# Kernel optimization log

Measured on AMD Instinct MI355X. Metric: run time of the kernel, lower is better.

## Reference

```python
import jax, jax.numpy as jnp
import numpy as np

N_EMBD = 1024
N_HEAD = 16
HEAD = N_EMBD // N_HEAD
B, T = 4, 2048


def setup_inputs() -> dict:
    key = jax.random.key(0)
    k1, k2, k3, k4, k5 = jax.random.split(key, 5)
    s = 1.0 / np.sqrt(N_EMBD)
    x = jax.random.normal(k1, (B, T, N_EMBD), dtype=jnp.float32)
    W_qkv = jax.random.uniform(k2, (N_EMBD, 3 * N_EMBD), jnp.float32, -s, s)
    b_qkv = jax.random.uniform(k3, (3 * N_EMBD,), jnp.float32, -s, s)
    W_out = jax.random.uniform(k4, (N_EMBD, N_EMBD), jnp.float32, -s, s)
    b_out = jax.random.uniform(k5, (N_EMBD,), jnp.float32, -s, s)
    return {"x": x, "W_qkv": W_qkv, "b_qkv": b_qkv, "W_out": W_out, "b_out": b_out}


def reference(x, W_qkv, b_qkv, W_out, b_out):
    Bx, Tx, C = x.shape
    qkv = x @ W_qkv + b_qkv                      # [B,T,3C]
    q, k, v = jnp.split(qkv, 3, axis=-1)
    def to_heads(t):
        return t.reshape(Bx, Tx, N_HEAD, HEAD).transpose(0, 2, 1, 3)  # [B,H,T,hd]
    q, k, v = to_heads(q), to_heads(k), to_heads(v)
    scores = jnp.einsum('bhqd,bhkd->bhqk', q, k) / np.sqrt(HEAD)
    causal = jnp.tril(jnp.ones((Tx, Tx), dtype=bool))
    scores = jnp.where(causal[None, None, :, :], scores, jnp.float32(-1e9))
    attn = jax.nn.softmax(scores, axis=-1)       # dropout p=0 (eval)
    out = jnp.einsum('bhqk,bhkd->bhqd', attn, v)
    out = out.transpose(0, 2, 1, 3).reshape(Bx, Tx, C)
    return out @ W_out + b_out
```

## Files before the change

kernel.cpp:

```cpp
#include <hip/hip_runtime.h>

typedef __attribute__((ext_vector_type(8))) short short8;
typedef __attribute__((ext_vector_type(8))) _Float16 half8;
typedef __attribute__((ext_vector_type(4))) float f32x4;
typedef __attribute__((ext_vector_type(16))) float f32x16;

#define MFMA_BF16(a, b, c) __builtin_amdgcn_mfma_f32_16x16x32_bf16(a, b, c, 0, 0, 0)
#define MFMA32_BF16(a, b, c) __builtin_amdgcn_mfma_f32_32x32x16_bf16(a, b, c, 0, 0, 0)
#define MFMA32_F16(a, b, c) __builtin_amdgcn_mfma_f32_32x32x16_f16(a, b, c, 0, 0, 0)

#define GLD16(g, l)                                                          \
  __builtin_amdgcn_global_load_lds(                                          \
      (const __attribute__((address_space(1))) unsigned int*)(g),            \
      (__attribute__((address_space(3))) unsigned int*)(l), 16, 0, 0)

__device__ __forceinline__ unsigned short f2bf(float f) {
  unsigned int u = __float_as_uint(f);
  u += 0x7fffu + ((u >> 16) & 1u);
  return (unsigned short)(u >> 16);
}

__global__ __launch_bounds__(256) void cvt_f32_bf16_k(const float* __restrict__ in,
                                                      unsigned short* __restrict__ out,
                                                      int n4) {
  int i = blockIdx.x * 256 + threadIdx.x;
  if (i < n4) {
    float4 v = reinterpret_cast<const float4*>(in)[i];
    ushort4 o;
    o.x = f2bf(v.x); o.y = f2bf(v.y); o.z = f2bf(v.z); o.w = f2bf(v.w);
    reinterpret_cast<ushort4*>(out)[i] = o;
  }
}

__global__ __launch_bounds__(256) void transpose_cvt_k(const float* __restrict__ W,
                                                       unsigned short* __restrict__ Wt,
                                                       int N) {
  __shared__ float tile[64][65];
  const int tid = threadIdx.x;
  const int tk = blockIdx.x * 64;
  const int tn = blockIdx.y * 64;
#pragma unroll
  for (int c = 0; c < 4; ++c) {
    int k = c * 16 + (tid >> 4);
    int n = (tid & 15) * 4;
    float4 v = *reinterpret_cast<const float4*>(&W[(size_t)(tk + k) * N + tn + n]);
    tile[k][n] = v.x; tile[k][n + 1] = v.y; tile[k][n + 2] = v.z; tile[k][n + 3] = v.w;
  }
  __syncthreads();
#pragma unroll
  for (int p = 0; p < 2; ++p) {
    int n = p * 32 + (tid >> 3);
    int k = (tid & 7) * 8;
    ushort4 a, b;
    a.x = f2bf(tile[k + 0][n]); a.y = f2bf(tile[k + 1][n]);
    a.z = f2bf(tile[k + 2][n]); a.w = f2bf(tile[k + 3][n]);
    b.x = f2bf(tile[k + 4][n]); b.y = f2bf(tile[k + 5][n]);
    b.z = f2bf(tile[k + 6][n]); b.w = f2bf(tile[k + 7][n]);
    *reinterpret_cast<ushort4*>(&Wt[(size_t)(tn + n) * 1024 + tk + k]) = a;
    *reinterpret_cast<ushort4*>(&Wt[(size_t)(tn + n) * 1024 + tk + k + 4]) = b;
  }
}

template <int MODE, int BN>
__global__ __launch_bounds__(256) void gemm_bt(const unsigned short* __restrict__ A,
                                               const unsigned short* __restrict__ Bt,
                                               const float* __restrict__ bias,
                                               float* __restrict__ outF,
                                               unsigned short* __restrict__ q_ws,
                                               unsigned short* __restrict__ k_ws,
                                               unsigned short* __restrict__ vt_ws,
                                               int M, int N, int K) {
  constexpr int NJ = BN / 32;
  constexpr int NBC = BN * 64 / 2048;
  __shared__ unsigned short As[128 * 64];
  __shared__ unsigned short Bs[BN * 64];

  const int tid = threadIdx.x;
  const int wave = tid >> 6, lane = tid & 63;
  const int quad = lane >> 4, l15 = lane & 15;
  const int m0 = blockIdx.x * 128, n0 = blockIdx.y * BN;
  const int wm = (wave & 1) * 64, wn = (wave >> 1) * (BN / 2);

  const f32x4 zf = {0.f, 0.f, 0.f, 0.f};
  f32x4 acc[4][NJ];
#pragma unroll
  for (int i = 0; i < 4; ++i)
#pragma unroll
    for (int j = 0; j < NJ; ++j) acc[i][j] = zf;

  const int rr = tid >> 3;
  const int scol = ((tid & 7) ^ (rr & 7)) * 8;
  const int swz = l15 & 7;

  for (int kt = 0; kt < K; kt += 64) {
    __syncthreads();
#pragma unroll
    for (int c = 0; c < 4; ++c)
      GLD16(&A[(size_t)(m0 + c * 32 + rr) * K + kt + scol], &As[c * 2048 + tid * 8]);
#pragma unroll
    for (int c = 0; c < NBC; ++c)
      GLD16(&Bt[(size_t)(n0 + c * 32 + rr) * K + kt + scol], &Bs[c * 2048 + tid * 8]);
    __syncthreads();

#pragma unroll
    for (int kk = 0; kk < 2; ++kk) {
      const int ch = (kk * 4 + quad) ^ swz;
      short8 af[4], bg[NJ];
#pragma unroll
      for (int i = 0; i < 4; ++i)
        af[i] = *reinterpret_cast<const short8*>(&As[(wm + i * 16 + l15) * 64 + ch * 8]);
#pragma unroll
      for (int j = 0; j < NJ; ++j)
        bg[j] = *reinterpret_cast<const short8*>(&Bs[(wn + j * 16 + l15) * 64 + ch * 8]);
#pragma unroll
      for (int i = 0; i < 4; ++i)
#pragma unroll
        for (int j = 0; j < NJ; ++j) acc[i][j] = MFMA_BF16(af[i], bg[j], acc[i][j]);
    }
  }

  const float kScQ = 0.125f * 1.44269504088896f;
  const int cls = n0 >> 10;
#pragma unroll
  for (int i = 0; i < 4; ++i) {
#pragma unroll
    for (int j = 0; j < NJ; ++j) {
      const int n = n0 + wn + j * 16 + l15;
      const float bv = bias[n];
      const int mb = m0 + wm + i * 16 + quad * 4;
      if (MODE == 1) {
#pragma unroll
        for (int r = 0; r < 4; ++r) outF[(size_t)(mb + r) * N + n] = acc[i][j][r] + bv;
      } else if (cls == 0) {
        const int b = mb >> 11, t0 = mb & 2047;
        const int h = n >> 6, d = n & 63;
#pragma unroll
        for (int r = 0; r < 4; ++r)
          q_ws[(((size_t)(b * 16 + h)) * 2048 + t0 + r) * 64 + d] =
              f2bf((acc[i][j][r] + bv) * kScQ);
      } else if (cls == 1) {
        const int b = mb >> 11, t0 = mb & 2047;
        const int n2 = n - 1024, h = n2 >> 6, d = n2 & 63;
#pragma unroll
        for (int r = 0; r < 4; ++r)
          k_ws[(((size_t)(b * 16 + h)) * 2048 + t0 + r) * 64 + d] = f2bf(acc[i][j][r] + bv);
      } else {
        const int b = mb >> 11, t0 = mb & 2047;
        const int n2 = n - 2048, h = n2 >> 6, d = n2 & 63;
        uint2 pk;
        pk.x = __builtin_bit_cast(unsigned int,
                                  __builtin_amdgcn_cvt_pkrtz(acc[i][j][0] + bv, acc[i][j][1] + bv));
        pk.y = __builtin_bit_cast(unsigned int,
                                  __builtin_amdgcn_cvt_pkrtz(acc[i][j][2] + bv, acc[i][j][3] + bv));
        *reinterpret_cast<uint2*>(
            &vt_ws[(((size_t)(b * 16 + h)) * 64 + d) * 2048 + t0]) = pk;
      }
    }
  }
}

__global__ __launch_bounds__(256, 3) void attn_k(const unsigned short* __restrict__ q_ws,
                                                 const unsigned short* __restrict__ k_ws,
                                                 const unsigned short* __restrict__ vt_ws,
                                                 unsigned short* __restrict__ att_ws) {
  const int T = 2048;
  const int bid = blockIdx.x;
  const int bh = (bid & 7) * 8 + ((bid >> 3) & 7);
  const int s = 15 - (bid >> 6);
  const int tid = threadIdx.x;
  const int wv = tid >> 6, lane = tid & 63;
  const int L = lane & 31, hl = lane >> 5;

  const unsigned short* Qh = q_ws + (size_t)bh * T * 64;
  const unsigned short* Kh = k_ws + (size_t)bh * T * 64;
  const _Float16* Vh = (const _Float16*)vt_ws + (size_t)bh * 64 * T;
  const int b = bh >> 4, h = bh & 15;

  __shared__ unsigned short Ks[2][64 * 64];
  __shared__ _Float16 Vs[2][64 * 64];
  __shared__ _Float16 plds_all[4][32 * 72];
  _Float16* plds = plds_all[wv];

  const int qw = s * 4 + wv;
  const int q0 = qw * 32;
  const int diagTile = qw >> 1;
  const int nk = 2 * s + 2;
  const int myq = q0 + L;

  short8 qb[4];
#pragma unroll
  for (int kk = 0; kk < 4; ++kk)
    qb[kk] = *reinterpret_cast<const short8*>(&Qh[(size_t)(q0 + L) * 64 + kk * 16 + hl * 8]);

  f32x16 o0 = {}, o1 = {};
  float l_i = 0.f;

  const int srow8 = tid >> 3;
  const int schunk = (tid & 7) ^ (srow8 & 7);

  GLD16(&Kh[(size_t)srow8 * 64 + schunk * 8], &Ks[0][tid * 8]);
  GLD16(&Kh[(size_t)(32 + srow8) * 64 + schunk * 8], &Ks[0][2048 + tid * 8]);
  GLD16(&Vh[(size_t)srow8 * T + schunk * 8], &Vs[0][tid * 8]);
  GLD16(&Vh[(size_t)(32 + srow8) * T + schunk * 8], &Vs[0][2048 + tid * 8]);

  for (int kt = 0; kt < nk; ++kt) {
    const int cur = kt & 1, nxt = cur ^ 1;
    if (kt) asm volatile("s_barrier" ::: "memory");
    const int pf = (kt + 1 < nk) ? kt + 1 : nk - 1;
    GLD16(&Kh[(size_t)(pf * 64 + srow8) * 64 + schunk * 8], &Ks[nxt][tid * 8]);
    GLD16(&Kh[(size_t)(pf * 64 + 32 + srow8) * 64 + schunk * 8], &Ks[nxt][2048 + tid * 8]);
    GLD16(&Vh[(size_t)srow8 * T + pf * 64 + schunk * 8], &Vs[nxt][tid * 8]);
    GLD16(&Vh[(size_t)(32 + srow8) * T + pf * 64 + schunk * 8], &Vs[nxt][2048 + tid * 8]);
    asm volatile("s_waitcnt vmcnt(4)\n\ts_barrier" ::: "memory");

    if (kt <= diagTile) {
      const unsigned short* KsC = Ks[cur];
      const _Float16* VsC = Vs[cur];
      const int kb = kt * 64;

      f32x16 sc0 = {}, sc1 = {};
#pragma unroll
      for (int kk = 0; kk < 4; ++kk) {
        const int sl = ((kk * 2 + hl) ^ (L & 7)) * 8;
        short8 k0 = *reinterpret_cast<const short8*>(&KsC[L * 64 + sl]);
        short8 k1 = *reinterpret_cast<const short8*>(&KsC[(32 + L) * 64 + sl]);
        sc0 = MFMA32_BF16(k0, qb[kk], sc0);
        sc1 = MFMA32_BF16(k1, qb[kk], sc1);
      }
      if (kt == diagTile) {
#pragma unroll
        for (int reg = 0; reg < 16; ++reg) {
          const int row = (reg & 3) + 8 * (reg >> 2) + 4 * hl;
          sc0[reg] = (kb + row > myq) ? -1e30f : sc0[reg];
          sc1[reg] = (kb + 32 + row > myq) ? -1e30f : sc1[reg];
        }
      }
#pragma unroll
      for (int c = 0; c < 2; ++c) {
        const f32x16& scc = c ? sc1 : sc0;
#pragma unroll
        for (int g = 0; g < 4; ++g) {
          float a0 = exp2f(scc[4 * g + 0]);
          float a1 = exp2f(scc[4 * g + 1]);
          float a2 = exp2f(scc[4 * g + 2]);
          float a3 = exp2f(scc[4 * g + 3]);
          l_i += (a0 + a1) + (a2 + a3);
          uint2 pk;
          pk.x = __builtin_bit_cast(unsigned int, __builtin_amdgcn_cvt_pkrtz(a0, a1));
          pk.y = __builtin_bit_cast(unsigned int, __builtin_amdgcn_cvt_pkrtz(a2, a3));
          *reinterpret_cast<uint2*>(&plds[L * 72 + c * 32 + g * 8 + hl * 4]) = pk;
        }
      }
      asm volatile("" ::: "memory");

#pragma unroll
      for (int t = 0; t < 4; ++t) {
        half8 pb = *reinterpret_cast<const half8*>(&plds[L * 72 + t * 16 + hl * 8]);
        const int sl = ((t * 2 + hl) ^ (L & 7)) * 8;
        half8 v0 = *reinterpret_cast<const half8*>(&VsC[L * 64 + sl]);
        half8 v1 = *reinterpret_cast<const half8*>(&VsC[(32 + L) * 64 + sl]);
        o0 = MFMA32_F16(v0, pb, o0);
        o1 = MFMA32_F16(v1, pb, o1);
      }
      asm volatile("" ::: "memory");
    }
  }
  asm volatile("s_waitcnt vmcnt(0)" ::: "memory");

  l_i += __shfl_xor(l_i, 32);
  const float inv = 1.f / l_i;
#pragma unroll
  for (int sg = 0; sg < 2; ++sg) {
    const f32x16& oo = sg ? o1 : o0;
#pragma unroll
    for (int g = 0; g < 4; ++g) {
      const int d0 = sg * 32 + g * 8 + hl * 4;
      uint2 ov;
      ov.x = (unsigned)f2bf(oo[4 * g + 0] * inv) | ((unsigned)f2bf(oo[4 * g + 1] * inv) << 16);
      ov.y = (unsigned)f2bf(oo[4 * g + 2] * inv) | ((unsigned)f2bf(oo[4 * g + 3] * inv) << 16);
      *reinterpret_cast<uint2*>(
          &att_ws[(size_t)(b * 2048 + q0 + L) * 1024 + h * 64 + d0]) = ov;
    }
  }
}

extern "C" void kernel_launch(void* const* d_in, const int* in_sizes, int n_in,
                              void* d_out, int out_size, void* d_ws, size_t ws_size,
                              hipStream_t stream) {
  (void)in_sizes; (void)n_in; (void)out_size; (void)ws_size;
  const float* x     = (const float*)d_in[0];
  const float* W_qkv = (const float*)d_in[1];
  const float* b_qkv = (const float*)d_in[2];
  const float* W_out = (const float*)d_in[3];
  const float* b_out = (const float*)d_in[4];
  float* out = (float*)d_out;

  char* ws = (char*)d_ws;
  unsigned short* xb    = (unsigned short*)(ws);
  unsigned short* wqkvT = (unsigned short*)(ws + 16777216);
  unsigned short* woutT = (unsigned short*)(ws + 23068672);
  unsigned short* q_ws  = (unsigned short*)(ws + 25165824);
  unsigned short* k_ws  = (unsigned short*)(ws + 41943040);
  unsigned short* vt_ws = (unsigned short*)(ws + 58720256);
  unsigned short* attb  = (unsigned short*)(ws + 75497472);

  cvt_f32_bf16_k<<<8192, 256, 0, stream>>>(x, xb, 2097152);
  transpose_cvt_k<<<dim3(16, 48), 256, 0, stream>>>(W_qkv, wqkvT, 3072);
  transpose_cvt_k<<<dim3(16, 16), 256, 0, stream>>>(W_out, woutT, 1024);

  dim3 g1(64, 24);
  gemm_bt<0, 128><<<g1, 256, 0, stream>>>(xb, wqkvT, b_qkv, nullptr, q_ws, k_ws, vt_ws,
                                          8192, 3072, 1024);
  attn_k<<<1024, 256, 0, stream>>>(q_ws, k_ws, vt_ws, attb);

  dim3 g2(64, 16);
  gemm_bt<1, 64><<<g2, 256, 0, stream>>>(attb, woutT, b_out, out, nullptr, nullptr, nullptr,
                                         8192, 1024, 1024);
}
```

Before: 241.1 us.

## Keep attention P in registers via permlane swap, interleave softmax with PV MFMAs, merge prep kernels

The attention kernel no longer writes P to a per-wave LDS buffer and reads it back. It uses v_permlane32_swap to rearrange the packed fp16 probabilities directly into the MFMA B-operand layout, and splits softmax and PV into two halves so V loads and MFMAs overlap with the exp work. It also adds s_setprio around the MFMA groups and packed f32 adds for the row sum. Separately, the three input conversion and transpose kernels are merged into one launch to cut launch overhead. The risk lies in the permlane layout correctness and higher register pressure.

```diff
diff --git a/kernel.cpp b/kernel.cpp
--- a/kernel.cpp
+++ b/kernel.cpp
@@ -4,6 +4,8 @@
 typedef __attribute__((ext_vector_type(8))) _Float16 half8;
 typedef __attribute__((ext_vector_type(4))) float f32x4;
 typedef __attribute__((ext_vector_type(16))) float f32x16;
+typedef __attribute__((ext_vector_type(4))) unsigned uint4v;
+typedef __attribute__((ext_vector_type(2))) float float2v;
 
 #define MFMA_BF16(a, b, c) __builtin_amdgcn_mfma_f32_16x16x32_bf16(a, b, c, 0, 0, 0)
 #define MFMA32_BF16(a, b, c) __builtin_amdgcn_mfma_f32_32x32x16_bf16(a, b, c, 0, 0, 0)
@@ -20,25 +22,30 @@
   return (unsigned short)(u >> 16);
 }
 
-__global__ __launch_bounds__(256) void cvt_f32_bf16_k(const float* __restrict__ in,
-                                                      unsigned short* __restrict__ out,
-                                                      int n4) {
-  int i = blockIdx.x * 256 + threadIdx.x;
-  if (i < n4) {
-    float4 v = reinterpret_cast<const float4*>(in)[i];
+__global__ __launch_bounds__(256) void prep_k(const float* __restrict__ x,
+                                              unsigned short* __restrict__ xb,
+                                              const float* __restrict__ W_qkv,
+                                              unsigned short* __restrict__ wqkvT,
+                                              const float* __restrict__ W_out,
+                                              unsigned short* __restrict__ woutT) {
+  __shared__ float tile[64][65];
+  const int blk = blockIdx.x;
+  const int tid = threadIdx.x;
+  if (blk < 8192) {
+    int i = blk * 256 + tid;
+    float4 v = reinterpret_cast<const float4*>(x)[i];
     ushort4 o;
     o.x = f2bf(v.x); o.y = f2bf(v.y); o.z = f2bf(v.z); o.w = f2bf(v.w);
-    reinterpret_cast<ushort4*>(out)[i] = o;
-  }
-}
-
-__global__ __launch_bounds__(256) void transpose_cvt_k(const float* __restrict__ W,
-                                                       unsigned short* __restrict__ Wt,
-                                                       int N) {
-  __shared__ float tile[64][65];
-  const int tid = threadIdx.x;
-  const int tk = blockIdx.x * 64;
-  const int tn = blockIdx.y * 64;
+    reinterpret_cast<ushort4*>(xb)[i] = o;
+    return;
+  }
+  const float* W;
+  unsigned short* Wt;
+  int N, bx;
+  if (blk < 8960) { W = W_qkv; Wt = wqkvT; N = 3072; bx = blk - 8192; }
+  else            { W = W_out; Wt = woutT; N = 1024; bx = blk - 8960; }
+  const int tk = (bx & 15) * 64;
+  const int tn = (bx >> 4) * 64;
 #pragma unroll
   for (int c = 0; c < 4; ++c) {
     int k = c * 16 + (tid >> 4);
@@ -178,8 +185,6 @@
 
   __shared__ unsigned short Ks[2][64 * 64];
   __shared__ _Float16 Vs[2][64 * 64];
-  __shared__ _Float16 plds_all[4][32 * 72];
-  _Float16* plds = plds_all[wv];
 
   const int qw = s * 4 + wv;
   const int q0 = qw * 32;
@@ -193,7 +198,7 @@
     qb[kk] = *reinterpret_cast<const short8*>(&Qh[(size_t)(q0 + L) * 64 + kk * 16 + hl * 8]);
 
   f32x16 o0 = {}, o1 = {};
-  float l_i = 0.f;
+  float2v li = {0.f, 0.f};
 
   const int srow8 = tid >> 3;
   const int schunk = (tid & 7) ^ (srow8 & 7);
@@ -202,6 +207,27 @@
   GLD16(&Kh[(size_t)(32 + srow8) * 64 + schunk * 8], &Ks[0][2048 + tid * 8]);
   GLD16(&Vh[(size_t)srow8 * T + schunk * 8], &Vs[0][tid * 8]);
   GLD16(&Vh[(size_t)(32 + srow8) * T + schunk * 8], &Vs[0][2048 + tid * 8]);
+
+  auto softmax32 = [&](const f32x16& scc, unsigned (&pwc)[4][2]) {
+#pragma unroll
+    for (int g = 0; g < 4; ++g) {
+      float2v e01, e23;
+      e01[0] = exp2f(scc[4 * g + 0]);
+      e01[1] = exp2f(scc[4 * g + 1]);
+      e23[0] = exp2f(scc[4 * g + 2]);
+      e23[1] = exp2f(scc[4 * g + 3]);
+      float2v s2;
+      asm("v_pk_add_f32 %0, %1, %2" : "=v"(s2) : "v"(e01), "v"(e23));
+      asm("v_pk_add_f32 %0, %0, %1" : "+v"(li) : "v"(s2));
+      pwc[g][0] = __builtin_bit_cast(unsigned int, __builtin_amdgcn_cvt_pkrtz(e01[0], e01[1]));
+      pwc[g][1] = __builtin_bit_cast(unsigned int, __builtin_amdgcn_cvt_pkrtz(e23[0], e23[1]));
+    }
+#pragma unroll
+    for (int r = 0; r < 2; ++r) {
+      asm volatile("v_permlane32_swap_b32 %0, %1" : "+v"(pwc[0][r]), "+v"(pwc[1][r]));
+      asm volatile("v_permlane32_swap_b32 %0, %1" : "+v"(pwc[2][r]), "+v"(pwc[3][r]));
+    }
+  };
 
   for (int kt = 0; kt < nk; ++kt) {
     const int cur = kt & 1, nxt = cur ^ 1;
@@ -219,6 +245,7 @@
       const int kb = kt * 64;
 
       f32x16 sc0 = {}, sc1 = {};
+      __builtin_amdgcn_s_setprio(1);
 #pragma unroll
       for (int kk = 0; kk < 4; ++kk) {
         const int sl = ((kk * 2 + hl) ^ (L & 7)) * 8;
@@ -227,46 +254,73 @@
         sc0 = MFMA32_BF16(k0, qb[kk], sc0);
         sc1 = MFMA32_BF16(k1, qb[kk], sc1);
       }
+      __builtin_amdgcn_s_setprio(0);
+
+      half8 vr0[2], vr1[2];
+#pragma unroll
+      for (int t = 0; t < 2; ++t) {
+        const int sl = ((t * 2 + hl) ^ (L & 7)) * 8;
+        vr0[t] = *reinterpret_cast<const half8*>(&VsC[L * 64 + sl]);
+        vr1[t] = *reinterpret_cast<const half8*>(&VsC[(32 + L) * 64 + sl]);
+      }
+
       if (kt == diagTile) {
 #pragma unroll
         for (int reg = 0; reg < 16; ++reg) {
           const int row = (reg & 3) + 8 * (reg >> 2) + 4 * hl;
           sc0[reg] = (kb + row > myq) ? -1e30f : sc0[reg];
+        }
+      }
+      unsigned pw0[4][2], pw1[4][2];
+      softmax32(sc0, pw0);
+
+      half8 vr2[2], vr3[2];
+#pragma unroll
+      for (int t = 2; t < 4; ++t) {
+        const int sl = ((t * 2 + hl) ^ (L & 7)) * 8;
+        vr2[t - 2] = *reinterpret_cast<const half8*>(&VsC[L * 64 + sl]);
+        vr3[t - 2] = *reinterpret_cast<const half8*>(&VsC[(32 + L) * 64 + sl]);
+      }
+
+      __builtin_amdgcn_s_setprio(1);
+      {
+        uint4v f0 = {pw0[0][0], pw0[0][1], pw0[1][0], pw0[1][1]};
+        uint4v f1 = {pw0[2][0], pw0[2][1], pw0[3][0], pw0[3][1]};
+        half8 pb0 = __builtin_bit_cast(half8, f0);
+        half8 pb1 = __builtin_bit_cast(half8, f1);
+        o0 = MFMA32_F16(vr0[0], pb0, o0);
+        o1 = MFMA32_F16(vr1[0], pb0, o1);
+        o0 = MFMA32_F16(vr0[1], pb1, o0);
+        o1 = MFMA32_F16(vr1[1], pb1, o1);
+      }
+      __builtin_amdgcn_s_setprio(0);
+
+      if (kt == diagTile) {
+#pragma unroll
+        for (int reg = 0; reg < 16; ++reg) {
+          const int row = (reg & 3) + 8 * (reg >> 2) + 4 * hl;
           sc1[reg] = (kb + 32 + row > myq) ? -1e30f : sc1[reg];
         }
       }
-#pragma unroll
-      for (int c = 0; c < 2; ++c) {
-        const f32x16& scc = c ? sc1 : sc0;
-#pragma unroll
-        for (int g = 0; g < 4; ++g) {
-          float a0 = exp2f(scc[4 * g + 0]);
-          float a1 = exp2f(scc[4 * g + 1]);
-          float a2 = exp2f(scc[4 * g + 2]);
-          float a3 = exp2f(scc[4 * g + 3]);
-          l_i += (a0 + a1) + (a2 + a3);
-          uint2 pk;
-          pk.x = __builtin_bit_cast(unsigned int, __builtin_amdgcn_cvt_pkrtz(a0, a1));
-          pk.y = __builtin_bit_cast(unsigned int, __builtin_amdgcn_cvt_pkrtz(a2, a3));
-          *reinterpret_cast<uint2*>(&plds[L * 72 + c * 32 + g * 8 + hl * 4]) = pk;
-        }
-      }
-      asm volatile("" ::: "memory");
-
-#pragma unroll
-      for (int t = 0; t < 4; ++t) {
-        half8 pb = *reinterpret_cast<const half8*>(&plds[L * 72 + t * 16 + hl * 8]);
-        const int sl = ((t * 2 + hl) ^ (L & 7)) * 8;
-        half8 v0 = *reinterpret_cast<const half8*>(&VsC[L * 64 + sl]);
-        half8 v1 = *reinterpret_cast<const half8*>(&VsC[(32 + L) * 64 + sl]);
-        o0 = MFMA32_F16(v0, pb, o0);
-        o1 = MFMA32_F16(v1, pb, o1);
-      }
-      asm volatile("" ::: "memory");
+      softmax32(sc1, pw1);
+
+      __builtin_amdgcn_s_setprio(1);
+      {
+        uint4v f0 = {pw1[0][0], pw1[0][1], pw1[1][0], pw1[1][1]};
+        uint4v f1 = {pw1[2][0], pw1[2][1], pw1[3][0], pw1[3][1]};
+        half8 pb0 = __builtin_bit_cast(half8, f0);
+        half8 pb1 = __builtin_bit_cast(half8, f1);
+        o0 = MFMA32_F16(vr2[0], pb0, o0);
+        o1 = MFMA32_F16(vr3[0], pb0, o1);
+        o0 = MFMA32_F16(vr2[1], pb1, o0);
+        o1 = MFMA32_F16(vr3[1], pb1, o1);
+      }
+      __builtin_amdgcn_s_setprio(0);
     }
   }
   asm volatile("s_waitcnt vmcnt(0)" ::: "memory");
 
+  float l_i = li[0] + li[1];
   l_i += __shfl_xor(l_i, 32);
   const float inv = 1.f / l_i;
 #pragma unroll
@@ -304,9 +358,7 @@
   unsigned short* vt_ws = (unsigned short*)(ws + 58720256);
   unsigned short* attb  = (unsigned short*)(ws + 75497472);
 
-  cvt_f32_bf16_k<<<8192, 256, 0, stream>>>(x, xb, 2097152);
-  transpose_cvt_k<<<dim3(16, 48), 256, 0, stream>>>(W_qkv, wqkvT, 3072);
-  transpose_cvt_k<<<dim3(16, 16), 256, 0, stream>>>(W_out, woutT, 1024);
+  prep_k<<<9216, 256, 0, stream>>>(x, xb, W_qkv, wqkvT, W_out, woutT);
 
   dim3 g1(64, 24);
   gemm_bt<0, 128><<<g1, 256, 0, stream>>>(xb, wqkvT, b_qkv, nullptr, q_ws, k_ws, vt_ws,
```

Result: slower. 247.9 us (+2.8%).
